# Kernel optimization log

Measured on AMD Instinct MI355X. Metric: run time of the kernel, lower is better.

The kernel has to match this reference:

```python
import jax, jax.numpy as jnp
import numpy as np

B, S, IN, D, H, L, F = 4, 1024, 6, 512, 8, 4, 2048
DK = D // H
EPS = 1e-5

def _pos_encoding(S, D):
    pos = np.arange(S, dtype=np.float32)[:, None]
    div = np.exp(np.arange(0, D, 2, dtype=np.float32) * (-np.log(10000.0) / D))
    pe = np.zeros((S, D), np.float32)
    pe[:, 0::2] = np.sin(pos * div)
    pe[:, 1::2] = np.cos(pos * div)
    return jnp.asarray(pe)

def setup_inputs() -> dict:
    key = jax.random.key(0)
    ks = jax.random.split(key, 12)
    def w(k, shape):
        return jax.random.normal(k, shape, jnp.float32) * 0.02
    return {
        "left_wrist": jax.random.normal(ks[0], (B, S, IN), jnp.float32),
        "right_wrist": jax.random.normal(ks[1], (B, S, IN), jnp.float32),
        "Wl": w(ks[2], (IN, D)), "bl": jnp.zeros((D,), jnp.float32),
        "Wr": w(ks[3], (IN, D)), "br": jnp.zeros((D,), jnp.float32),
        "pe": _pos_encoding(S, D),
        # 4 attention blocks per layer (cross1to2, cross2to1, self1, self2), each with q/k/v/o projections
        "mha_w": w(ks[4], (L, 4, 4, D, D)), "mha_b": jnp.zeros((L, 4, 4, D), jnp.float32),
        "mha_ln_g": jnp.ones((L, 4, D), jnp.float32), "mha_ln_b": jnp.zeros((L, 4, D), jnp.float32),
        # 2 FFNs per layer (channel 1 / channel 2)
        "ff_w1": w(ks[5], (L, 2, D, F)), "ff_b1": jnp.zeros((L, 2, F), jnp.float32),
        "ff_w2": w(ks[6], (L, 2, F, D)), "ff_b2": jnp.zeros((L, 2, D), jnp.float32),
        "ff_ln_g": jnp.ones((L, 2, D), jnp.float32), "ff_ln_b": jnp.zeros((L, 2, D), jnp.float32),
        "h1_w1": w(ks[7], (2 * D, D)), "h1_b1": jnp.zeros((D,), jnp.float32),
        "h1_w2": w(ks[8], (D, 2)), "h1_b2": jnp.zeros((2,), jnp.float32),
        "h2_w1": w(ks[9], (2 * D, D)), "h2_b1": jnp.zeros((D,), jnp.float32),
        "h2_w2": w(ks[10], (D, 2)), "h2_b2": jnp.zeros((2,), jnp.float32),
    }

def _ln(x, g, b):
    m = jnp.mean(x, axis=-1, keepdims=True)
    v = jnp.var(x, axis=-1, keepdims=True)
    return (x - m) * jax.lax.rsqrt(v + EPS) * g + b

def _mha(q_in, k_in, v_in, w, b, g, beta):
    # w: [4, D, D] for q/k/v/o, b: [4, D]
    def proj(x, i):
        return (x @ w[i] + b[i]).reshape(x.shape[0], x.shape[1], H, DK).transpose(0, 2, 1, 3)
    Q, K, V = proj(q_in, 0), proj(k_in, 1), proj(v_in, 2)
    scores = jnp.einsum('bhqd,bhkd->bhqk', Q, K) * np.float32(1.0 / np.sqrt(DK))
    attn = jax.nn.softmax(scores, axis=-1)
    ctx = jnp.einsum('bhqk,bhkd->bhqd', attn, V)
    ctx = ctx.transpose(0, 2, 1, 3).reshape(q_in.shape[0], q_in.shape[1], D)
    out = ctx @ w[3] + b[3]
    return _ln(out + q_in, g, beta)

def _ffn(x, w1, b1, w2, b2, g, beta):
    h = jax.nn.relu(x @ w1 + b1)
    return _ln(h @ w2 + b2 + x, g, beta)

def reference(left_wrist, right_wrist, Wl, bl, Wr, br, pe,
              mha_w, mha_b, mha_ln_g, mha_ln_b,
              ff_w1, ff_b1, ff_w2, ff_b2, ff_ln_g, ff_ln_b,
              h1_w1, h1_b1, h1_w2, h1_b2, h2_w1, h2_b1, h2_w2, h2_b2):
    left = left_wrist @ Wl + bl + pe[None]
    right = right_wrist @ Wr + br + pe[None]
    for l in range(L):
        lc = _mha(left, right, right, mha_w[l, 0], mha_b[l, 0], mha_ln_g[l, 0], mha_ln_b[l, 0])
        rc = _mha(right, left, left, mha_w[l, 1], mha_b[l, 1], mha_ln_g[l, 1], mha_ln_b[l, 1])
        ls = _mha(lc, lc, lc, mha_w[l, 2], mha_b[l, 2], mha_ln_g[l, 2], mha_ln_b[l, 2])
        rs = _mha(rc, rc, rc, mha_w[l, 3], mha_b[l, 3], mha_ln_g[l, 3], mha_ln_b[l, 3])
        left = _ffn(ls, ff_w1[l, 0], ff_b1[l, 0], ff_w2[l, 0], ff_b2[l, 0], ff_ln_g[l, 0], ff_ln_b[l, 0])
        right = _ffn(rs, ff_w1[l, 1], ff_b1[l, 1], ff_w2[l, 1], ff_b2[l, 1], ff_ln_g[l, 1], ff_ln_b[l, 1])
    # AdaptiveAvgPool1d(1) over seq == mean over seq axis
    fused = jnp.concatenate([jnp.mean(left, axis=1), jnp.mean(right, axis=1)], axis=1)  # [B, 2D]
    logits1 = jax.nn.relu(fused @ h1_w1 + h1_b1) @ h1_w2 + h1_b2
    logits2 = jax.nn.relu(fused @ h2_w1 + h2_b1) @ h2_w2 + h2_b2
    return (logits1, logits2)
```

## Files before the change

### kernel.cpp

```cpp
#include <hip/hip_runtime.h>
#include <hip/hip_bf16.h>

#define NB 4
#define NS 1024
#define NIN 6
#define ND 512
#define NH 8
#define NLAYERS 4
#define NF 2048
#define NDK 64
#define LN_EPS 1e-5f

typedef unsigned short u16;
typedef __attribute__((ext_vector_type(4))) unsigned short u16x4;
typedef __attribute__((ext_vector_type(8))) short s16x8;
typedef __attribute__((ext_vector_type(4))) float f32x4;
typedef __attribute__((ext_vector_type(4))) unsigned int u32x4;

#define MFMA_BF16(A, B, C) __builtin_amdgcn_mfma_f32_16x16x32_bf16(A, B, C, 0, 0, 0)

#define GLOAD_LDS16(gsrc, ldst)                                                  \
    __builtin_amdgcn_global_load_lds(                                            \
        (const __attribute__((address_space(1))) void*)(gsrc),                   \
        (__attribute__((address_space(3))) void*)(ldst), 16, 0, 0)

__device__ inline u16 f2bf(float f) {
    __bf16 h = (__bf16)f;
    return __builtin_bit_cast(u16, h);
}
__device__ inline float bf2f(u16 v) {
    unsigned int u = (unsigned int)v << 16;
    return __builtin_bit_cast(float, u);
}

__global__ __launch_bounds__(256) void transpose_kernel(
    const float* __restrict__ src, u16* __restrict__ dst, int K, int N) {
    __shared__ u16 t[64][72];
    const int tid = threadIdx.x;
    src += (size_t)blockIdx.z * K * N;
    dst += (size_t)blockIdx.z * K * N;
    const int n0 = blockIdx.x * 64, k0 = blockIdx.y * 64;
    {
        int r = tid >> 2, cq = (tid & 3) * 16;
        const float* sp = src + (size_t)(k0 + r) * N + n0 + cq;
#pragma unroll
        for (int q = 0; q < 4; ++q) {
            float4 v = *reinterpret_cast<const float4*>(sp + q * 4);
            t[r][cq + q * 4 + 0] = f2bf(v.x);
            t[r][cq + q * 4 + 1] = f2bf(v.y);
            t[r][cq + q * 4 + 2] = f2bf(v.z);
            t[r][cq + q * 4 + 3] = f2bf(v.w);
        }
    }
    __syncthreads();
    {
        int rn = tid >> 2, cq = (tid & 3) * 16;
        s16x8 o0, o1;
#pragma unroll
        for (int j = 0; j < 8; ++j) o0[j] = (short)t[cq + j][rn];
#pragma unroll
        for (int j = 0; j < 8; ++j) o1[j] = (short)t[cq + 8 + j][rn];
        u16* dp = dst + (size_t)(n0 + rn) * K + k0 + cq;
        *reinterpret_cast<s16x8*>(dp) = o0;
        *reinterpret_cast<s16x8*>(dp + 8) = o1;
    }
}

__global__ __launch_bounds__(256) void in_proj_kernel(
    const float* __restrict__ x, const float* __restrict__ W,
    const float* __restrict__ bias, const float* __restrict__ pe,
    float* __restrict__ out, u16* __restrict__ outb) {
    int idx = blockIdx.x * 256 + threadIdx.x;
    int d = idx & (ND - 1);
    int bs = idx / ND;
    int s = bs & (NS - 1);
    const float* xr = x + (size_t)bs * NIN;
    float acc = bias[d] + pe[(size_t)s * ND + d];
#pragma unroll
    for (int i = 0; i < NIN; ++i) acc += xr[i] * W[(size_t)i * ND + d];
    out[idx] = acc;
    outb[idx] = f2bf(acc);
}

template <int BN>
__device__ inline void gemm_core(const u16* __restrict__ A, const u16* __restrict__ Wt,
                                 int K, int bm, int bn, char* lds, int tid,
                                 f32x4 (&acc)[4][BN / 32]) {
    constexpr int NT = BN / 32;
    constexpr int ASZ = 128 * 128;
    constexpr int BSZ = BN * 128;
    const int wid = tid >> 6, lane = tid & 63;
    const int l15 = lane & 15, lhi = lane >> 4;
    const int wr = wid >> 1, wc = wid & 1;

    auto stage = [&](int buf, int k0) {
#pragma unroll
        for (int i = 0; i < 4; ++i) {
            int slot = (wid * 4 + i) * 64 + lane;
            int r = slot >> 3, p = slot & 7;
            const char* src = (const char*)(A + (size_t)(bm + r) * K + k0)
                              + ((p * 16) ^ ((r & 7) << 4));
            GLOAD_LDS16(src, lds + buf * ASZ + (wid * 4 + i) * 1024);
        }
#pragma unroll
        for (int i = 0; i < BN / 32; ++i) {
            int slot = (wid * (BN / 32) + i) * 64 + lane;
            int r = slot >> 3, p = slot & 7;
            const char* src = (const char*)(Wt + (size_t)(bn + r) * K + k0)
                              + ((p * 16) ^ ((r & 7) << 4));
            GLOAD_LDS16(src, lds + 2 * ASZ + buf * BSZ + (wid * (BN / 32) + i) * 1024);
        }
    };

#pragma unroll
    for (int mt = 0; mt < 4; ++mt)
#pragma unroll
        for (int nt = 0; nt < NT; ++nt) acc[mt][nt] = f32x4{0.f, 0.f, 0.f, 0.f};

    const int KT = K >> 6;
    stage(0, 0);
    __syncthreads();
    for (int t = 0; t < KT; ++t) {
        if (t + 1 < KT) stage((t + 1) & 1, (t + 1) << 6);
        const char* Ab = lds + (t & 1) * ASZ;
        const char* Bb = lds + 2 * ASZ + (t & 1) * BSZ;
#pragma unroll
        for (int sl = 0; sl < 2; ++sl) {
            s16x8 af[4];
#pragma unroll
            for (int mt = 0; mt < 4; ++mt) {
                int row = wr * 64 + mt * 16 + l15;
                af[mt] = *reinterpret_cast<const s16x8*>(
                    Ab + ((row * 128 + sl * 64 + lhi * 16) ^ ((row & 7) << 4)));
            }
            s16x8 bfr[NT];
#pragma unroll
            for (int nt = 0; nt < NT; ++nt) {
                int row = wc * (BN / 2) + nt * 16 + l15;
                bfr[nt] = *reinterpret_cast<const s16x8*>(
                    Bb + ((row * 128 + sl * 64 + lhi * 16) ^ ((row & 7) << 4)));
            }
#pragma unroll
            for (int mt = 0; mt < 4; ++mt)
#pragma unroll
                for (int nt = 0; nt < NT; ++nt)
                    acc[mt][nt] = MFMA_BF16(af[mt], bfr[nt], acc[mt][nt]);
        }
        __syncthreads();
    }
}

template <int OMODE, int BN>
__global__ __launch_bounds__(256) void bgemm2_kernel(
    const u16* __restrict__ a0, const u16* __restrict__ a1,
    const u16* __restrict__ wt0, const u16* __restrict__ wt1,
    const float* __restrict__ bias0, const float* __restrict__ bias1,
    u16* __restrict__ Cv, int M, int N, int K) {
    constexpr int NT = BN / 32;
    __shared__ char lds[2 * 128 * 128 + 2 * BN * 128];
    const int tid = threadIdx.x, z = blockIdx.z;
    const int bm = blockIdx.y * 128, bn = blockIdx.x * BN;
    const u16* A = z ? a1 : a0;
    const u16* Wt = z ? wt1 : wt0;
    const float* bias = z ? bias1 : bias0;

    f32x4 acc[4][NT];
    gemm_core<BN>(A, Wt, K, bm, bn, lds, tid, acc);

    const int wid = tid >> 6, lane = tid & 63;
    const int l15 = lane & 15, lhi = lane >> 4;
    const int wr = wid >> 1, wc = wid & 1;
    float bv[NT];
#pragma unroll
    for (int nt = 0; nt < NT; ++nt) bv[nt] = bias[bn + wc * (BN / 2) + nt * 16 + l15];

    u16* C = Cv + (size_t)z * M * N;
#pragma unroll
    for (int mt = 0; mt < 4; ++mt) {
        int m0 = bm + wr * 64 + mt * 16 + lhi * 4;
#pragma unroll
        for (int nt = 0; nt < NT; ++nt) {
            int n = bn + wc * (BN / 2) + nt * 16 + l15;
#pragma unroll
            for (int r = 0; r < 4; ++r) {
                float v = acc[mt][nt][r] + bv[nt];
                if (OMODE == 1) v = fmaxf(v, 0.f);
                C[(size_t)(m0 + r) * N + n] = f2bf(v);
            }
        }
    }
}

__global__ __launch_bounds__(256) void bgemm_qkv_kernel(
    const u16* __restrict__ aq0, const u16* __restrict__ aq1,
    const u16* __restrict__ akv0, const u16* __restrict__ akv1,
    const u16* __restrict__ wt0, const u16* __restrict__ wt1,
    const float* __restrict__ bb0, const float* __restrict__ bb1,
    u16* __restrict__ Qo, u16* __restrict__ Ko, u16* __restrict__ Vto) {
    __shared__ char lds[2 * 128 * 128 + 2 * 64 * 128];
    const int tid = threadIdx.x, z = blockIdx.z;
    const int proj = blockIdx.x >> 3;
    const int bm = blockIdx.y * 128, bn = (blockIdx.x & 7) * 64;
    const int M = NB * NS;
    const u16* A = (proj == 0) ? (z ? aq1 : aq0) : (z ? akv1 : akv0);
    const u16* Wt = (z ? wt1 : wt0) + (size_t)proj * ND * ND;
    const float* bias = (z ? bb1 : bb0) + proj * ND;

    f32x4 acc[4][2];
    gemm_core<64>(A, Wt, ND, bm, bn, lds, tid, acc);

    const int wid = tid >> 6, lane = tid & 63;
    const int l15 = lane & 15, lhi = lane >> 4;
    const int wr = wid >> 1, wc = wid & 1;
    float bv[2];
#pragma unroll
    for (int nt = 0; nt < 2; ++nt) bv[nt] = bias[bn + wc * 32 + nt * 16 + l15];

    if (proj < 2) {
        u16* C = (proj ? Ko : Qo) + (size_t)z * M * ND;
#pragma unroll
        for (int mt = 0; mt < 4; ++mt) {
            int m0 = bm + wr * 64 + mt * 16 + lhi * 4;
#pragma unroll
            for (int nt = 0; nt < 2; ++nt) {
                int n = bn + wc * 32 + nt * 16 + l15;
#pragma unroll
                for (int r = 0; r < 4; ++r)
                    C[(size_t)(m0 + r) * ND + n] = f2bf(acc[mt][nt][r] + bv[nt]);
            }
        }
    } else {
#pragma unroll
        for (int mt = 0; mt < 4; ++mt) {
            int m0 = bm + wr * 64 + mt * 16 + lhi * 4;
            int b = (z * M + m0) >> 10, s = m0 & (NS - 1);
#pragma unroll
            for (int nt = 0; nt < 2; ++nt) {
                int n = bn + wc * 32 + nt * 16 + l15;
                int h = n >> 6, dk = n & 63;
                u16x4 o = {f2bf(acc[mt][nt][0] + bv[nt]), f2bf(acc[mt][nt][1] + bv[nt]),
                           f2bf(acc[mt][nt][2] + bv[nt]), f2bf(acc[mt][nt][3] + bv[nt])};
                *reinterpret_cast<u16x4*>(Vto + ((size_t)((b * NH + h) * NDK + dk)) * NS + s) = o;
            }
        }
    }
}

__global__ __launch_bounds__(256) void ln2_kernel(
    const u16* __restrict__ x, const float* __restrict__ res,
    const float* __restrict__ g0, const float* __restrict__ g1,
    const float* __restrict__ be0, const float* __restrict__ be1,
    float* __restrict__ outf, u16* __restrict__ outb) {
    int row = blockIdx.x;
    const float* g = (row >> 12) ? g1 : g0;
    const float* be = (row >> 12) ? be1 : be0;
    int tid = threadIdx.x;
    unsigned int xp = *reinterpret_cast<const unsigned int*>(x + (size_t)row * ND + tid * 2);
    float2 rr = *reinterpret_cast<const float2*>(res + (size_t)row * ND + tid * 2);
    float v0 = bf2f((u16)(xp & 0xffffu)) + rr.x;
    float v1 = bf2f((u16)(xp >> 16)) + rr.y;
    float s = v0 + v1, sq = v0 * v0 + v1 * v1;
#pragma unroll
    for (int m = 1; m < 64; m <<= 1) { s += __shfl_xor(s, m); sq += __shfl_xor(sq, m); }
    __shared__ float ls[4], lq[4];
    int wid = tid >> 6, lane = tid & 63;
    if (lane == 0) { ls[wid] = s; lq[wid] = sq; }
    __syncthreads();
    s = ls[0] + ls[1] + ls[2] + ls[3];
    sq = lq[0] + lq[1] + lq[2] + lq[3];
    float mean = s * (1.f / ND);
    float var = sq * (1.f / ND) - mean * mean;
    float rstd = rsqrtf(var + LN_EPS);
    float2 gg = *reinterpret_cast<const float2*>(g + tid * 2);
    float2 bb = *reinterpret_cast<const float2*>(be + tid * 2);
    float o0 = (v0 - mean) * rstd * gg.x + bb.x;
    float o1 = (v1 - mean) * rstd * gg.y + bb.y;
    float2 of = {o0, o1};
    *reinterpret_cast<float2*>(outf + (size_t)row * ND + tid * 2) = of;
    unsigned int ob = (unsigned int)f2bf(o0) | ((unsigned int)f2bf(o1) << 16);
    *reinterpret_cast<unsigned int*>(outb + (size_t)row * ND + tid * 2) = ob;
}

__global__ __launch_bounds__(256) void attn_kernel(
    const u16* __restrict__ Qb, const u16* __restrict__ Kb,
    const u16* __restrict__ Vtb, u16* __restrict__ O) {
    __shared__ u16 Ks[128 * 64];
    __shared__ u16 Vts[64 * 128];
    __shared__ u16 Ps[4][16 * 128];

    const int tid = threadIdx.x;
    const int w = tid >> 6, lane = tid & 63;
    const int l15 = lane & 15, lhi = lane >> 4;
    const int bh = blockIdx.y;
    const int b = bh >> 3, h = bh & 7;
    const int qb = blockIdx.x * 64 + w * 16;
    const float c1 = 0.18033688011f;

    s16x8 qf[2];
    {
        const u16* qp = Qb + ((size_t)(b * NS) + qb + l15) * ND + h * NDK + lhi * 8;
        qf[0] = *reinterpret_cast<const s16x8*>(qp);
        qf[1] = *reinterpret_cast<const s16x8*>(qp + 32);
    }

    f32x4 o[4] = {f32x4{0.f, 0.f, 0.f, 0.f}, f32x4{0.f, 0.f, 0.f, 0.f},
                  f32x4{0.f, 0.f, 0.f, 0.f}, f32x4{0.f, 0.f, 0.f, 0.f}};
    float m = -1e30f;
    float lsum = 0.f;

    const u16* Kbase = Kb + ((size_t)(b * NS)) * ND + h * NDK;
    const u16* Vbase = Vtb + ((size_t)bh * NDK) * NS;

    for (int c = 0; c < NS / 128; ++c) {
        const int kv0 = c * 128;
        __syncthreads();
#pragma unroll
        for (int i = 0; i < 4; ++i) {
            int slot = (w * 4 + i) * 64 + lane;
            {
                int r = slot >> 3, p = slot & 7;
                const char* src = (const char*)(Kbase + (size_t)(kv0 + r) * ND)
                                  + ((p ^ (r & 7)) * 16);
                GLOAD_LDS16(src, (char*)Ks + (w * 4 + i) * 1024);
            }
            {
                int r = slot >> 4, p = slot & 15;
                const char* src = (const char*)(Vbase + (size_t)r * NS + kv0)
                                  + ((p ^ (r & 7)) * 16);
                GLOAD_LDS16(src, (char*)Vts + (w * 4 + i) * 1024);
            }
        }
        __syncthreads();

        f32x4 sc[8];
#pragma unroll
        for (int blk = 0; blk < 8; ++blk) sc[blk] = f32x4{0.f, 0.f, 0.f, 0.f};
#pragma unroll
        for (int sl = 0; sl < 2; ++sl) {
#pragma unroll
            for (int blk = 0; blk < 8; ++blk) {
                int krow = blk * 16 + l15;
                s16x8 kf = *reinterpret_cast<const s16x8*>((char*)Ks +
                    ((krow * 128 + sl * 64 + lhi * 16) ^ ((krow & 7) << 4)));
                sc[blk] = MFMA_BF16(kf, qf[sl], sc[blk]);
            }
        }
        float mx = -1e30f;
#pragma unroll
        for (int blk = 0; blk < 8; ++blk)
#pragma unroll
            for (int r = 0; r < 4; ++r) mx = fmaxf(mx, sc[blk][r]);
        mx = fmaxf(mx, __shfl_xor(mx, 16));
        mx = fmaxf(mx, __shfl_xor(mx, 32));
        float mn = fmaxf(m, mx);
        float corr = exp2f((m - mn) * c1);
        m = mn;
        float d = mn * c1;
        float rs = 0.f;
#pragma unroll
        for (int blk = 0; blk < 8; ++blk) {
#pragma unroll
            for (int r = 0; r < 4; ++r) {
                float p = exp2f(fmaf(sc[blk][r], c1, -d));
                sc[blk][r] = p;
                rs += p;
            }
        }
        rs += __shfl_xor(rs, 16);
        rs += __shfl_xor(rs, 32);
        lsum = lsum * corr + rs;
#pragma unroll
        for (int blk = 0; blk < 8; ++blk) {
            u16x4 pk = {f2bf(sc[blk][0]), f2bf(sc[blk][1]),
                        f2bf(sc[blk][2]), f2bf(sc[blk][3])};
            *reinterpret_cast<u16x4*>((char*)(Ps[w]) +
                ((l15 * 256 + blk * 32 + lhi * 8) ^ ((l15 & 7) << 4))) = pk;
        }
        float cO[4];
#pragma unroll
        for (int r = 0; r < 4; ++r) cO[r] = __shfl(corr, lhi * 4 + r);
#pragma unroll
        for (int db = 0; db < 4; ++db)
#pragma unroll
            for (int r = 0; r < 4; ++r) o[db][r] *= cO[r];
#pragma unroll
        for (int sl2 = 0; sl2 < 4; ++sl2) {
            s16x8 pf = *reinterpret_cast<const s16x8*>((char*)(Ps[w]) +
                ((l15 * 256 + sl2 * 64 + lhi * 16) ^ ((l15 & 7) << 4)));
#pragma unroll
            for (int db = 0; db < 4; ++db) {
                int vr = db * 16 + l15;
                s16x8 vf = *reinterpret_cast<const s16x8*>((char*)Vts +
                    ((vr * 256 + sl2 * 64 + lhi * 16) ^ ((vr & 7) << 4)));
                o[db] = MFMA_BF16(pf, vf, o[db]);
            }
        }
    }
    float lsO[4];
#pragma unroll
    for (int r = 0; r < 4; ++r) lsO[r] = __shfl(lsum, lhi * 4 + r);
#pragma unroll
    for (int db = 0; db < 4; ++db) {
#pragma unroll
        for (int r = 0; r < 4; ++r) {
            int q = qb + lhi * 4 + r;
            O[((size_t)(b * NS) + q) * ND + h * NDK + db * 16 + l15] =
                f2bf(o[db][r] / lsO[r]);
        }
    }
}

__global__ __launch_bounds__(256) void pool2_kernel(
    const float* __restrict__ RES, float* __restrict__ fused) {
    const int b = blockIdx.x, half = blockIdx.y, sc = blockIdx.z;
    const size_t NTOK = (size_t)NB * NS * ND;
    const float* src = RES + (half ? NTOK : 0) + ((size_t)(b * NS + sc * 128)) * ND;
    const int tid = threadIdx.x;
#pragma unroll
    for (int cc = 0; cc < 2; ++cc) {
        int c = cc * 256 + tid;
        float s = 0.f;
        for (int r = 0; r < 128; ++r) s += src[(size_t)r * ND + c];
        atomicAdd(&fused[b * 1024 + half * 512 + c], s * (1.f / NS));
    }
}

__global__ __launch_bounds__(256) void head_hidden_kernel(
    const float* __restrict__ fused,
    const float* __restrict__ w1a, const float* __restrict__ b1a,
    const float* __restrict__ w1b, const float* __restrict__ b1b,
    float* __restrict__ hid) {
    const int b = blockIdx.x >> 1, head = blockIdx.x & 1;
    const float* w1 = head ? w1b : w1a;
    const float* b1 = head ? b1b : b1a;
    const int tid = threadIdx.x;
    const int j = blockIdx.y * 64 + (tid & 63);
    const int kq = tid >> 6;
    const float* fr = fused + (size_t)b * (2 * ND);
    float p = 0.f;
    for (int k = kq * 256; k < kq * 256 + 256; ++k)
        p += fr[k] * w1[(size_t)k * ND + j];
    __shared__ float part[4][64];
    part[kq][tid & 63] = p;
    __syncthreads();
    if (tid < 64) {
        float v = part[0][tid] + part[1][tid] + part[2][tid] + part[3][tid] + b1[j];
        hid[(size_t)blockIdx.x * ND + j] = fmaxf(v, 0.f);
    }
}

__global__ __launch_bounds__(256) void head_out_kernel(
    const float* __restrict__ hid,
    const float* __restrict__ w2a, const float* __restrict__ b2a,
    const float* __restrict__ w2b, const float* __restrict__ b2b,
    float* __restrict__ out) {
    const int b = blockIdx.x >> 1, head = blockIdx.x & 1;
    const float* w2 = head ? w2b : w2a;
    const float* b2 = head ? b2b : b2a;
    const int tid = threadIdx.x;
    const float* hr = hid + (size_t)blockIdx.x * ND;
    float h0 = hr[tid], h1 = hr[tid + 256];
    float p0 = h0 * w2[tid * 2 + 0] + h1 * w2[(tid + 256) * 2 + 0];
    float p1 = h0 * w2[tid * 2 + 1] + h1 * w2[(tid + 256) * 2 + 1];
#pragma unroll
    for (int m = 1; m < 64; m <<= 1) { p0 += __shfl_xor(p0, m); p1 += __shfl_xor(p1, m); }
    __shared__ float r0s[4], r1s[4];
    int wid = tid >> 6, lane = tid & 63;
    if (lane == 0) { r0s[wid] = p0; r1s[wid] = p1; }
    __syncthreads();
    if (tid == 0) {
        out[head * 8 + b * 2 + 0] = r0s[0] + r0s[1] + r0s[2] + r0s[3] + b2[0];
        out[head * 8 + b * 2 + 1] = r1s[0] + r1s[1] + r1s[2] + r1s[3] + b2[1];
    }
}

extern "C" void kernel_launch(void* const* d_in, const int* in_sizes, int n_in,
                              void* d_out, int out_size, void* d_ws, size_t ws_size,
                              hipStream_t stream) {
    const float* left_wrist  = (const float*)d_in[0];
    const float* right_wrist = (const float*)d_in[1];
    const float* Wl = (const float*)d_in[2];
    const float* bl = (const float*)d_in[3];
    const float* Wr = (const float*)d_in[4];
    const float* br = (const float*)d_in[5];
    const float* pe = (const float*)d_in[6];
    const float* mha_w    = (const float*)d_in[7];
    const float* mha_b    = (const float*)d_in[8];
    const float* mha_ln_g = (const float*)d_in[9];
    const float* mha_ln_b = (const float*)d_in[10];
    const float* ff_w1 = (const float*)d_in[11];
    const float* ff_b1 = (const float*)d_in[12];
    const float* ff_w2 = (const float*)d_in[13];
    const float* ff_b2 = (const float*)d_in[14];
    const float* ff_ln_g = (const float*)d_in[15];
    const float* ff_ln_b = (const float*)d_in[16];
    const float* h1_w1 = (const float*)d_in[17];
    const float* h1_b1 = (const float*)d_in[18];
    const float* h1_w2 = (const float*)d_in[19];
    const float* h1_b2 = (const float*)d_in[20];
    const float* h2_w1 = (const float*)d_in[21];
    const float* h2_b1 = (const float*)d_in[22];
    const float* h2_w2 = (const float*)d_in[23];
    const float* h2_b2 = (const float*)d_in[24];
    float* out = (float*)d_out;

    const size_t NTOK = (size_t)NB * NS * ND;
    const int M = NB * NS;
    float* ws = (float*)d_ws;
    float* RES   = ws;
    float* CRES  = RES + 2 * NTOK;
    float* TMPf  = CRES + 2 * NTOK;
    float* FUSED = TMPf + 2 * NTOK;
    float* HID   = FUSED + NB * 2 * ND;
    u16* TMPbf = (u16*)TMPf;
    u16* Xbf  = (u16*)(HID + 8 * ND);
    u16* CXbf = Xbf + 2 * NTOK;
    u16* Qbf  = CXbf + 2 * NTOK;
    u16* Kbf  = Qbf + 2 * NTOK;
    u16* Vtbf = Kbf + 2 * NTOK;
    u16* CTbf = Vtbf + 2 * NTOK;
    u16* Hh   = Qbf;
    u16* WtM  = CTbf + 2 * NTOK;
    u16* WtF1 = WtM + (size_t)64 * ND * ND;
    u16* WtF2 = WtF1 + (size_t)8 * ND * NF;

    const size_t DD = (size_t)ND * ND;

    transpose_kernel<<<dim3(ND / 64, ND / 64, 64), 256, 0, stream>>>(mha_w, WtM, ND, ND);
    transpose_kernel<<<dim3(NF / 64, ND / 64, 8), 256, 0, stream>>>(ff_w1, WtF1, ND, NF);
    transpose_kernel<<<dim3(ND / 64, NF / 64, 8), 256, 0, stream>>>(ff_w2, WtF2, NF, ND);

    in_proj_kernel<<<(NB * NS * ND) / 256, 256, 0, stream>>>(left_wrist, Wl, bl, pe, RES, Xbf);
    in_proj_kernel<<<(NB * NS * ND) / 256, 256, 0, stream>>>(right_wrist, Wr, br, pe,
                                                             RES + NTOK, Xbf + NTOK);

    for (int l = 0; l < NLAYERS; ++l) {
        const u16* wt0 = WtM + ((size_t)l * 4 + 0) * 4 * DD;
        const u16* wt1 = WtM + ((size_t)l * 4 + 1) * 4 * DD;
        const u16* wt2 = WtM + ((size_t)l * 4 + 2) * 4 * DD;
        const u16* wt3 = WtM + ((size_t)l * 4 + 3) * 4 * DD;
        const float* bb0 = mha_b + ((size_t)l * 4 + 0) * 4 * ND;
        const float* bb1 = mha_b + ((size_t)l * 4 + 1) * 4 * ND;
        const float* bb2 = mha_b + ((size_t)l * 4 + 2) * 4 * ND;
        const float* bb3 = mha_b + ((size_t)l * 4 + 3) * 4 * ND;

        bgemm_qkv_kernel<<<dim3(24, 32, 2), 256, 0, stream>>>(
            Xbf, Xbf + NTOK, Xbf + NTOK, Xbf, wt0, wt1, bb0, bb1, Qbf, Kbf, Vtbf);
        attn_kernel<<<dim3(NS / 64, 2 * NB * NH), 256, 0, stream>>>(Qbf, Kbf, Vtbf, CTbf);
        bgemm2_kernel<2, 64><<<dim3(8, 32, 2), 256, 0, stream>>>(
            CTbf, CTbf + NTOK, wt0 + 3 * DD, wt1 + 3 * DD, bb0 + 3 * ND, bb1 + 3 * ND,
            TMPbf, M, ND, ND);
        ln2_kernel<<<2 * M, 256, 0, stream>>>(
            TMPbf, RES, mha_ln_g + ((size_t)l * 4 + 0) * ND, mha_ln_g + ((size_t)l * 4 + 1) * ND,
            mha_ln_b + ((size_t)l * 4 + 0) * ND, mha_ln_b + ((size_t)l * 4 + 1) * ND,
            CRES, CXbf);

        bgemm_qkv_kernel<<<dim3(24, 32, 2), 256, 0, stream>>>(
            CXbf, CXbf + NTOK, CXbf, CXbf + NTOK, wt2, wt3, bb2, bb3, Qbf, Kbf, Vtbf);
        attn_kernel<<<dim3(NS / 64, 2 * NB * NH), 256, 0, stream>>>(Qbf, Kbf, Vtbf, CTbf);
        bgemm2_kernel<2, 64><<<dim3(8, 32, 2), 256, 0, stream>>>(
            CTbf, CTbf + NTOK, wt2 + 3 * DD, wt3 + 3 * DD, bb2 + 3 * ND, bb3 + 3 * ND,
            TMPbf, M, ND, ND);
        ln2_kernel<<<2 * M, 256, 0, stream>>>(
            TMPbf, CRES, mha_ln_g + ((size_t)l * 4 + 2) * ND, mha_ln_g + ((size_t)l * 4 + 3) * ND,
            mha_ln_b + ((size_t)l * 4 + 2) * ND, mha_ln_b + ((size_t)l * 4 + 3) * ND,
            RES, Xbf);

        bgemm2_kernel<1, 128><<<dim3(16, 32, 2), 256, 0, stream>>>(
            Xbf, Xbf + NTOK, WtF1 + ((size_t)l * 2 + 0) * ND * NF, WtF1 + ((size_t)l * 2 + 1) * ND * NF,
            ff_b1 + ((size_t)l * 2 + 0) * NF, ff_b1 + ((size_t)l * 2 + 1) * NF,
            Hh, M, NF, ND);
        bgemm2_kernel<2, 64><<<dim3(8, 32, 2), 256, 0, stream>>>(
            Hh, Hh + (size_t)M * NF, WtF2 + ((size_t)l * 2 + 0) * NF * ND, WtF2 + ((size_t)l * 2 + 1) * NF * ND,
            ff_b2 + ((size_t)l * 2 + 0) * ND, ff_b2 + ((size_t)l * 2 + 1) * ND,
            TMPbf, M, ND, NF);
        ln2_kernel<<<2 * M, 256, 0, stream>>>(
            TMPbf, RES, ff_ln_g + ((size_t)l * 2 + 0) * ND, ff_ln_g + ((size_t)l * 2 + 1) * ND,
            ff_ln_b + ((size_t)l * 2 + 0) * ND, ff_ln_b + ((size_t)l * 2 + 1) * ND,
            RES, Xbf);
    }

    hipMemsetAsync(FUSED, 0, NB * 2 * ND * sizeof(float), stream);
    pool2_kernel<<<dim3(NB, 2, 8), 256, 0, stream>>>(RES, FUSED);
    head_hidden_kernel<<<dim3(8, 8), 256, 0, stream>>>(FUSED, h1_w1, h1_b1, h2_w1, h2_b1, HID);
    head_out_kernel<<<8, 256, 0, stream>>>(HID, h1_w2, h1_b2, h2_w2, h2_b2, out);
}
```

Before: 1.351 ms.

## Use one wave per row in LayerNorm and add lazy softmax rescaling in attention

LayerNorm now assigns one 64-lane wave per row with 8 elements per lane and 128-bit loads, which removes the shared-memory reduction and block barrier and launches a quarter as many blocks. The attention kernel only rescales the output accumulator and running sum when the running max grows by more than a threshold, so the exp and multiply work is skipped on most tiles. It also splits the P staging into two halves, halving the LDS used for P, and adds a launch-bounds occupancy hint. Skipping the rescale lets the softmax exponentials grow up to 2^8 before rescaling, which is safe in fp32 but slightly changes rounding.

```diff
diff --git a/kernel.cpp b/kernel.cpp
--- a/kernel.cpp
+++ b/kernel.cpp
@@ -251,42 +251,62 @@
     const float* __restrict__ g0, const float* __restrict__ g1,
     const float* __restrict__ be0, const float* __restrict__ be1,
     float* __restrict__ outf, u16* __restrict__ outb) {
-    int row = blockIdx.x;
+    const int wid = threadIdx.x >> 6, lane = threadIdx.x & 63;
+    const int row = blockIdx.x * 4 + wid;
     const float* g = (row >> 12) ? g1 : g0;
     const float* be = (row >> 12) ? be1 : be0;
-    int tid = threadIdx.x;
-    unsigned int xp = *reinterpret_cast<const unsigned int*>(x + (size_t)row * ND + tid * 2);
-    float2 rr = *reinterpret_cast<const float2*>(res + (size_t)row * ND + tid * 2);
-    float v0 = bf2f((u16)(xp & 0xffffu)) + rr.x;
-    float v1 = bf2f((u16)(xp >> 16)) + rr.y;
-    float s = v0 + v1, sq = v0 * v0 + v1 * v1;
+    const int c0 = lane * 8;
+    const size_t base = (size_t)row * ND + c0;
+
+    u32x4 xp = *reinterpret_cast<const u32x4*>(x + base);
+    float4 ra = *reinterpret_cast<const float4*>(res + base);
+    float4 rb = *reinterpret_cast<const float4*>(res + base + 4);
+    float v[8];
+    v[0] = bf2f((u16)(xp[0] & 0xffffu)) + ra.x;
+    v[1] = bf2f((u16)(xp[0] >> 16)) + ra.y;
+    v[2] = bf2f((u16)(xp[1] & 0xffffu)) + ra.z;
+    v[3] = bf2f((u16)(xp[1] >> 16)) + ra.w;
+    v[4] = bf2f((u16)(xp[2] & 0xffffu)) + rb.x;
+    v[5] = bf2f((u16)(xp[2] >> 16)) + rb.y;
+    v[6] = bf2f((u16)(xp[3] & 0xffffu)) + rb.z;
+    v[7] = bf2f((u16)(xp[3] >> 16)) + rb.w;
+
+    float s = 0.f, sq = 0.f;
+#pragma unroll
+    for (int i = 0; i < 8; ++i) { s += v[i]; sq += v[i] * v[i]; }
 #pragma unroll
     for (int m = 1; m < 64; m <<= 1) { s += __shfl_xor(s, m); sq += __shfl_xor(sq, m); }
-    __shared__ float ls[4], lq[4];
-    int wid = tid >> 6, lane = tid & 63;
-    if (lane == 0) { ls[wid] = s; lq[wid] = sq; }
-    __syncthreads();
-    s = ls[0] + ls[1] + ls[2] + ls[3];
-    sq = lq[0] + lq[1] + lq[2] + lq[3];
     float mean = s * (1.f / ND);
     float var = sq * (1.f / ND) - mean * mean;
     float rstd = rsqrtf(var + LN_EPS);
-    float2 gg = *reinterpret_cast<const float2*>(g + tid * 2);
-    float2 bb = *reinterpret_cast<const float2*>(be + tid * 2);
-    float o0 = (v0 - mean) * rstd * gg.x + bb.x;
-    float o1 = (v1 - mean) * rstd * gg.y + bb.y;
-    float2 of = {o0, o1};
-    *reinterpret_cast<float2*>(outf + (size_t)row * ND + tid * 2) = of;
-    unsigned int ob = (unsigned int)f2bf(o0) | ((unsigned int)f2bf(o1) << 16);
-    *reinterpret_cast<unsigned int*>(outb + (size_t)row * ND + tid * 2) = ob;
-}
-
-__global__ __launch_bounds__(256) void attn_kernel(
+
+    float4 ga = *reinterpret_cast<const float4*>(g + c0);
+    float4 gb = *reinterpret_cast<const float4*>(g + c0 + 4);
+    float4 ba = *reinterpret_cast<const float4*>(be + c0);
+    float4 bb = *reinterpret_cast<const float4*>(be + c0 + 4);
+    float gg[8] = {ga.x, ga.y, ga.z, ga.w, gb.x, gb.y, gb.z, gb.w};
+    float bbv[8] = {ba.x, ba.y, ba.z, ba.w, bb.x, bb.y, bb.z, bb.w};
+    float o[8];
+#pragma unroll
+    for (int i = 0; i < 8; ++i) o[i] = (v[i] - mean) * rstd * gg[i] + bbv[i];
+
+    float4 oa = {o[0], o[1], o[2], o[3]};
+    float4 ob = {o[4], o[5], o[6], o[7]};
+    *reinterpret_cast<float4*>(outf + base) = oa;
+    *reinterpret_cast<float4*>(outf + base + 4) = ob;
+    u32x4 pk;
+#pragma unroll
+    for (int i = 0; i < 4; ++i)
+        pk[i] = (unsigned int)f2bf(o[2 * i]) | ((unsigned int)f2bf(o[2 * i + 1]) << 16);
+    *reinterpret_cast<u32x4*>(outb + base) = pk;
+}
+
+__global__ __launch_bounds__(256, 4) void attn_kernel(
     const u16* __restrict__ Qb, const u16* __restrict__ Kb,
     const u16* __restrict__ Vtb, u16* __restrict__ O) {
     __shared__ u16 Ks[128 * 64];
     __shared__ u16 Vts[64 * 128];
-    __shared__ u16 Ps[4][16 * 128];
+    __shared__ u16 Ps[4][16 * 64];
 
     const int tid = threadIdx.x;
     const int w = tid >> 6, lane = tid & 63;
@@ -353,9 +373,19 @@
         mx = fmaxf(mx, __shfl_xor(mx, 16));
         mx = fmaxf(mx, __shfl_xor(mx, 32));
         float mn = fmaxf(m, mx);
-        float corr = exp2f((m - mn) * c1);
-        m = mn;
-        float d = mn * c1;
+        if (__any((mn - m) * c1 > 8.f)) {
+            float corr = exp2f((m - mn) * c1);
+            m = mn;
+            lsum *= corr;
+            float cO[4];
+#pragma unroll
+            for (int r = 0; r < 4; ++r) cO[r] = __shfl(corr, lhi * 4 + r);
+#pragma unroll
+            for (int db = 0; db < 4; ++db)
+#pragma unroll
+                for (int r = 0; r < 4; ++r) o[db][r] *= cO[r];
+        }
+        float d = m * c1;
         float rs = 0.f;
 #pragma unroll
         for (int blk = 0; blk < 8; ++blk) {
@@ -368,31 +398,30 @@
         }
         rs += __shfl_xor(rs, 16);
         rs += __shfl_xor(rs, 32);
-        lsum = lsum * corr + rs;
-#pragma unroll
-        for (int blk = 0; blk < 8; ++blk) {
-            u16x4 pk = {f2bf(sc[blk][0]), f2bf(sc[blk][1]),
-                        f2bf(sc[blk][2]), f2bf(sc[blk][3])};
-            *reinterpret_cast<u16x4*>((char*)(Ps[w]) +
-                ((l15 * 256 + blk * 32 + lhi * 8) ^ ((l15 & 7) << 4))) = pk;
-        }
-        float cO[4];
-#pragma unroll
-        for (int r = 0; r < 4; ++r) cO[r] = __shfl(corr, lhi * 4 + r);
-#pragma unroll
-        for (int db = 0; db < 4; ++db)
-#pragma unroll
-            for (int r = 0; r < 4; ++r) o[db][r] *= cO[r];
-#pragma unroll
-        for (int sl2 = 0; sl2 < 4; ++sl2) {
-            s16x8 pf = *reinterpret_cast<const s16x8*>((char*)(Ps[w]) +
-                ((l15 * 256 + sl2 * 64 + lhi * 16) ^ ((l15 & 7) << 4)));
-#pragma unroll
-            for (int db = 0; db < 4; ++db) {
-                int vr = db * 16 + l15;
-                s16x8 vf = *reinterpret_cast<const s16x8*>((char*)Vts +
-                    ((vr * 256 + sl2 * 64 + lhi * 16) ^ ((vr & 7) << 4)));
-                o[db] = MFMA_BF16(pf, vf, o[db]);
+        lsum += rs;
+
+#pragma unroll
+        for (int hh = 0; hh < 2; ++hh) {
+#pragma unroll
+            for (int bl = 0; bl < 4; ++bl) {
+                int blk = hh * 4 + bl;
+                u16x4 pk = {f2bf(sc[blk][0]), f2bf(sc[blk][1]),
+                            f2bf(sc[blk][2]), f2bf(sc[blk][3])};
+                *reinterpret_cast<u16x4*>((char*)(Ps[w]) +
+                    ((l15 * 128 + bl * 32 + lhi * 8) ^ ((l15 & 7) << 4))) = pk;
+            }
+#pragma unroll
+            for (int sl2 = 0; sl2 < 2; ++sl2) {
+                s16x8 pf = *reinterpret_cast<const s16x8*>((char*)(Ps[w]) +
+                    ((l15 * 128 + sl2 * 64 + lhi * 16) ^ ((l15 & 7) << 4)));
+                int ss = hh * 2 + sl2;
+#pragma unroll
+                for (int db = 0; db < 4; ++db) {
+                    int vr = db * 16 + l15;
+                    s16x8 vf = *reinterpret_cast<const s16x8*>((char*)Vts +
+                        ((vr * 256 + ss * 64 + lhi * 16) ^ ((vr & 7) << 4)));
+                    o[db] = MFMA_BF16(pf, vf, o[db]);
+                }
             }
         }
     }
@@ -550,7 +579,7 @@
         bgemm2_kernel<2, 64><<<dim3(8, 32, 2), 256, 0, stream>>>(
             CTbf, CTbf + NTOK, wt0 + 3 * DD, wt1 + 3 * DD, bb0 + 3 * ND, bb1 + 3 * ND,
             TMPbf, M, ND, ND);
-        ln2_kernel<<<2 * M, 256, 0, stream>>>(
+        ln2_kernel<<<2 * M / 4, 256, 0, stream>>>(
             TMPbf, RES, mha_ln_g + ((size_t)l * 4 + 0) * ND, mha_ln_g + ((size_t)l * 4 + 1) * ND,
             mha_ln_b + ((size_t)l * 4 + 0) * ND, mha_ln_b + ((size_t)l * 4 + 1) * ND,
             CRES, CXbf);
@@ -561,7 +590,7 @@
         bgemm2_kernel<2, 64><<<dim3(8, 32, 2), 256, 0, stream>>>(
             CTbf, CTbf + NTOK, wt2 + 3 * DD, wt3 + 3 * DD, bb2 + 3 * ND, bb3 + 3 * ND,
             TMPbf, M, ND, ND);
-        ln2_kernel<<<2 * M, 256, 0, stream>>>(
+        ln2_kernel<<<2 * M / 4, 256, 0, stream>>>(
             TMPbf, CRES, mha_ln_g + ((size_t)l * 4 + 2) * ND, mha_ln_g + ((size_t)l * 4 + 3) * ND,
             mha_ln_b + ((size_t)l * 4 + 2) * ND, mha_ln_b + ((size_t)l * 4 + 3) * ND,
             RES, Xbf);
@@ -574,7 +603,7 @@
             Hh, Hh + (size_t)M * NF, WtF2 + ((size_t)l * 2 + 0) * NF * ND, WtF2 + ((size_t)l * 2 + 1) * NF * ND,
             ff_b2 + ((size_t)l * 2 + 0) * ND, ff_b2 + ((size_t)l * 2 + 1) * ND,
             TMPbf, M, ND, NF);
-        ln2_kernel<<<2 * M, 256, 0, stream>>>(
+        ln2_kernel<<<2 * M / 4, 256, 0, stream>>>(
             TMPbf, RES, ff_ln_g + ((size_t)l * 2 + 0) * ND, ff_ln_g + ((size_t)l * 2 + 1) * ND,
             ff_ln_b + ((size_t)l * 2 + 0) * ND, ff_ln_b + ((size_t)l * 2 + 1) * ND,
             RES, Xbf);
```

New measurement: 1.320 ms. 1.02x faster.
